# Performance work log

Hardware: AMD Instinct MI355X
Metric: run time of the kernel (lower is better)

## Reference

```python
import jax, jax.numpy as jnp
import numpy as np

H = 512
V = 32000
B = 64
S = 64
T = 64
SOS = 0


def setup_inputs() -> dict:
    key = jax.random.key(0)
    ks = jax.random.split(key, 20)
    s = 1.0 / np.sqrt(H)
    return {
        "encoder_outputs": jax.random.normal(ks[0], (B, S, H), jnp.float32),
        "encoder_hidden": jax.random.normal(ks[1], (1, B, H), jnp.float32),
        "target_tensor": jax.random.randint(ks[2], (B, T), 0, V),
        "emb": jax.random.normal(ks[3], (V, H), jnp.float32) * s,
        "Wa": jax.random.normal(ks[4], (H, H), jnp.float32) * s,
        "ba": jnp.zeros((H,), jnp.float32),
        "Ua": jax.random.normal(ks[5], (H, H), jnp.float32) * s,
        "bu": jnp.zeros((H,), jnp.float32),
        "Va": jax.random.normal(ks[6], (1, H), jnp.float32) * s,
        "bv": jnp.zeros((1,), jnp.float32),
        "W_ih": jax.random.normal(ks[7], (3 * H, 2 * H), jnp.float32) * s,
        "W_hh": jax.random.normal(ks[8], (3 * H, H), jnp.float32) * s,
        "b_ih": jnp.zeros((3 * H,), jnp.float32),
        "b_hh": jnp.zeros((3 * H,), jnp.float32),
        "W_out": jax.random.normal(ks[9], (V, H), jnp.float32) * s,
        "b_out": jnp.zeros((V,), jnp.float32),
    }


def reference(encoder_outputs, encoder_hidden, target_tensor, emb, Wa, ba, Ua, bu,
              Va, bv, W_ih, W_hh, b_ih, b_hh, W_out, b_out):
    # Teacher-forced inputs: SOS then target[:, :-1]
    sos = jnp.full((B, 1), SOS, dtype=target_tensor.dtype)
    inputs = jnp.concatenate([sos, target_tensor[:, :-1]], axis=1)  # [B,T]
    emb_seq = emb[inputs]  # [B,T,H]

    # Precompute Ua(keys): invariant across decode steps
    Uk = jnp.einsum('bsh,kh->bsk', encoder_outputs, Ua) + bu  # [B,S,H]
    h0 = encoder_hidden[0]  # [B,H]

    def step(h, x_t):
        # Bahdanau attention: Va * tanh(Wa q + Ua k)
        q = h @ Wa.T + ba                                   # [B,H]
        scores = jnp.tanh(q[:, None, :] + Uk) @ Va[0] + bv[0]  # [B,S]
        w = jax.nn.softmax(scores, axis=-1)                 # [B,S]
        ctx = jnp.einsum('bs,bsh->bh', w, encoder_outputs)  # [B,H]
        # GRU cell (PyTorch gate layout: r, z, n)
        x = jnp.concatenate([x_t, ctx], axis=-1)            # [B,2H]
        gi = x @ W_ih.T + b_ih
        gh = h @ W_hh.T + b_hh
        ir, iz, inn = jnp.split(gi, 3, axis=-1)
        hr, hz, hn = jnp.split(gh, 3, axis=-1)
        r = jax.nn.sigmoid(ir + hr)
        z = jax.nn.sigmoid(iz + hz)
        n = jnp.tanh(inn + r * hn)
        h_new = (1.0 - z) * n + z * h
        logits = h_new @ W_out.T + b_out                    # [B,V]
        return h_new, (logits, w)

    hT, (logits, attn) = jax.lax.scan(step, h0, jnp.swapaxes(emb_seq, 0, 1))
    log_probs = jax.nn.log_softmax(jnp.swapaxes(logits, 0, 1), axis=-1)  # [B,T,V]
    attentions = jnp.swapaxes(attn, 0, 1)                                # [B,T,S]
    return log_probs, hT[None], attentions
```

## Files before the change

### kernel.cpp

```cpp
#include <hip/hip_runtime.h>
#include <math.h>

#define HH 512
#define VV 32000
#define BB 64
#define SS 64
#define TT 64
#define H3 1536

#define WS_GIEMBBF 0LL
#define WS_UKBF    3145728LL
#define WS_ENCBF   4194304LL
#define WS_EMBBF   5242880LL
#define WS_WCATBF  6291456LL
#define WS_WIHC3   6815744LL
#define WS_WIHE    7208960LL
#define WS_UABF    7602176LL
#define WS_BCAT    7733248LL
#define WS_QGH     7735296LL
#define WS_CTXBF   7866368LL
#define WS_H32     7882752LL
#define WS_HBF     7948288LL
#define WS_HSALL   8388608LL

#define OUT_HT  ((long long)BB*TT*VV)
#define OUT_ATT (OUT_HT + (long long)BB*HH)

typedef __attribute__((ext_vector_type(8))) short bf16x8;
typedef __attribute__((ext_vector_type(4))) float f32x4;

__device__ inline unsigned short f2b(float x) {
  unsigned u = __builtin_bit_cast(unsigned, x);
  unsigned r = (u + 0x7FFF + ((u >> 16) & 1)) >> 16;
  return (unsigned short)r;
}
__device__ inline float bc(unsigned u) { return __builtin_bit_cast(float, u); }
__device__ inline float b2f(unsigned short h) { return bc(((unsigned)h) << 16); }
__device__ inline float frcp(float x) { return __builtin_amdgcn_rcpf(x); }
__device__ inline float tanh_fast(float x) { return 1.f - 2.f * frcp(__expf(2.f * x) + 1.f); }
__device__ inline float sigm(float x) { return frcp(1.f + __expf(-x)); }

#define GLDS(gp, lp) __builtin_amdgcn_global_load_lds( \
    (const __attribute__((address_space(1))) void*)(gp), \
    (__attribute__((address_space(3))) void*)(lp), 16, 0, 0)

__global__ __launch_bounds__(256) void build_wcat_kernel(const float* __restrict__ Wa,
    const float* __restrict__ Whh, const float* __restrict__ ba,
    const float* __restrict__ bhh, unsigned short* __restrict__ wcatbf,
    float* __restrict__ bcat)
{
  long long i = (long long)blockIdx.x * 256 + threadIdx.x;
  int j = (int)(i >> 9), k = (int)(i & 511);
  float v = (j < HH) ? Wa[(long long)j*HH + k] : Whh[(long long)(j - HH)*HH + k];
  wcatbf[i] = f2b(v);
  if (i < 2048) bcat[i] = (i < HH) ? ba[i] : bhh[i - HH];
}

__global__ __launch_bounds__(256) void build_wihc3_kernel(const float* __restrict__ W_ih,
    unsigned short* __restrict__ o)
{
  long long i = (long long)blockIdx.x * 256 + threadIdx.x;
  int rp = (int)(i >> 9), k = (int)(i & 511);
  int j = rp / 3, g = rp - j * 3;
  o[i] = f2b(W_ih[((long long)(g*512 + j))*1024 + 512 + k]);
}

__global__ __launch_bounds__(256) void build_wihe_kernel(const float* __restrict__ W_ih,
    unsigned short* __restrict__ o)
{
  long long i = (long long)blockIdx.x * 256 + threadIdx.x;
  o[i] = f2b(W_ih[(long long)(i >> 9)*1024 + (i & 511)]);
}

__global__ __launch_bounds__(256) void cvt_f2b_kernel(const float* __restrict__ in,
    unsigned short* __restrict__ outp, long long n)
{
  long long i = ((long long)blockIdx.x * 256 + threadIdx.x) * 4;
  if (i >= n) return;
  float4 v = *(const float4*)(in + i);
  ushort4 r = { f2b(v.x), f2b(v.y), f2b(v.z), f2b(v.w) };
  *(ushort4*)(outp + i) = r;
}

__global__ __launch_bounds__(256) void build_embbf_kernel(const float* __restrict__ emb,
    const int* __restrict__ tgt, unsigned short* __restrict__ embbf)
{
  const int m = blockIdx.x, t = m >> 6, b = m & 63;
  const int tk = (t == 0) ? 0 : tgt[b*TT + t - 1];
  const float* src = emb + (long long)tk*HH;
  unsigned short* dst = embbf + (long long)m*HH;
  const int i = threadIdx.x;
  dst[i] = f2b(src[i]);
  dst[i + 256] = f2b(src[i + 256]);
}

__global__ __launch_bounds__(256) void hinit_kernel(const float* __restrict__ eh,
    unsigned short* __restrict__ hbf0, float* __restrict__ h320)
{
  int i = blockIdx.x * 256 + threadIdx.x;
  float v = eh[i];
  hbf0[i] = f2b(v);
  h320[i] = v;
}

template<int OUTBF>
__global__ __launch_bounds__(256) void mfma_nt(const unsigned short* __restrict__ A,
    const unsigned short* __restrict__ Bw, const float* __restrict__ bias,
    void* __restrict__ Cv, long long ldc)
{
  __shared__ unsigned short As[128*32];
  __shared__ unsigned short Bs[128*32];
  const int tid = threadIdx.x;
  const int w = tid >> 6, l = tid & 63;
  const int m0 = blockIdx.y * 128, n0 = blockIdx.x * 128;
  const int wr = w >> 1, wc = w & 1;

  f32x4 acc[4][4];
  #pragma unroll
  for (int i = 0; i < 4; i++)
    #pragma unroll
    for (int j = 0; j < 4; j++) acc[i][j] = (f32x4){0.f, 0.f, 0.f, 0.f};

  const int srow = l >> 2;
  const int scol = (l & 3) * 8;

  for (int k0 = 0; k0 < HH; k0 += 32) {
    __syncthreads();
    #pragma unroll
    for (int q = 0; q < 2; ++q) {
      int r = w*32 + q*16 + srow;
      GLDS(A  + (long long)(m0 + r)*HH + k0 + scol, As + r*32 + scol);
      GLDS(Bw + (long long)(n0 + r)*HH + k0 + scol, Bs + r*32 + scol);
    }
    __syncthreads();

    bf16x8 a[4], b[4];
    #pragma unroll
    for (int mi = 0; mi < 4; mi++)
      a[mi] = *(const bf16x8*)&As[(wr*64 + mi*16 + (l & 15))*32 + (l >> 4)*8];
    #pragma unroll
    for (int ni = 0; ni < 4; ni++)
      b[ni] = *(const bf16x8*)&Bs[(wc*64 + ni*16 + (l & 15))*32 + (l >> 4)*8];
    #pragma unroll
    for (int mi = 0; mi < 4; mi++)
      #pragma unroll
      for (int ni = 0; ni < 4; ni++)
        acc[mi][ni] = __builtin_amdgcn_mfma_f32_16x16x32_bf16(a[mi], b[ni], acc[mi][ni], 0, 0, 0);
  }

  #pragma unroll
  for (int mi = 0; mi < 4; mi++) {
    #pragma unroll
    for (int ni = 0; ni < 4; ni++) {
      int col = n0 + wc*64 + ni*16 + (l & 15);
      float bb = bias[col];
      #pragma unroll
      for (int r2 = 0; r2 < 4; r2++) {
        int row = m0 + wr*64 + mi*16 + (l >> 4)*4 + r2;
        float v = acc[mi][ni][r2] + bb;
        if (OUTBF) ((unsigned short*)Cv)[(long long)row*ldc + col] = f2b(v);
        else       ((float*)Cv)[(long long)row*ldc + col] = v;
      }
    }
  }
}

__global__ __launch_bounds__(256) void qgh_mfma(
    const unsigned short* __restrict__ hbf_r, const unsigned short* __restrict__ wcatbf,
    const float* __restrict__ bcat, float* __restrict__ qgh)
{
  __shared__ unsigned short As[64*32];
  __shared__ unsigned short Bs[128*32];
  const int tid = threadIdx.x;
  const int w = tid >> 6, l = tid & 63;
  const int n0 = blockIdx.x * 128;
  const int wr = w >> 1, wc = w & 1;

  f32x4 acc[2][4];
  #pragma unroll
  for (int i = 0; i < 2; i++)
    #pragma unroll
    for (int j = 0; j < 4; j++) acc[i][j] = (f32x4){0.f, 0.f, 0.f, 0.f};

  const int ar = tid >> 2;
  const int ac8 = (tid & 3) * 8;

  for (int k0 = 0; k0 < HH; k0 += 32) {
    __syncthreads();
    GLDS(hbf_r + (long long)ar*HH + k0 + ac8, As + ar*32 + ac8);
    #pragma unroll
    for (int q = 0; q < 2; ++q) {
      int r = q*64 + ar;
      GLDS(wcatbf + (long long)(n0 + r)*HH + k0 + ac8, Bs + r*32 + ac8);
    }
    __syncthreads();

    bf16x8 a[2], b[4];
    #pragma unroll
    for (int mi = 0; mi < 2; mi++)
      a[mi] = *(const bf16x8*)&As[(wr*32 + mi*16 + (l & 15))*32 + (l >> 4)*8];
    #pragma unroll
    for (int ni = 0; ni < 4; ni++)
      b[ni] = *(const bf16x8*)&Bs[(wc*64 + ni*16 + (l & 15))*32 + (l >> 4)*8];
    #pragma unroll
    for (int mi = 0; mi < 2; mi++)
      #pragma unroll
      for (int ni = 0; ni < 4; ni++)
        acc[mi][ni] = __builtin_amdgcn_mfma_f32_16x16x32_bf16(a[mi], b[ni], acc[mi][ni], 0, 0, 0);
  }

  #pragma unroll
  for (int mi = 0; mi < 2; mi++) {
    #pragma unroll
    for (int ni = 0; ni < 4; ni++) {
      int col = n0 + wc*64 + ni*16 + (l & 15);
      float bb = bcat[col];
      #pragma unroll
      for (int r2 = 0; r2 < 4; r2++) {
        int row = wr*32 + mi*16 + (l >> 4)*4 + r2;
        qgh[(long long)row*2048 + col] = acc[mi][ni][r2] + bb;
      }
    }
  }
}

__global__ __launch_bounds__(512) void attn_kernel(int t,
    const float* __restrict__ qgh, const unsigned short* __restrict__ ukbf,
    const unsigned short* __restrict__ encbf, const float* __restrict__ Va,
    const float* __restrict__ bvp,
    unsigned short* __restrict__ ctxbf, float* __restrict__ attn_out)
{
  const int b = blockIdx.x, tid = threadIdx.x;
  __shared__ float qs2[8][68];
  __shared__ float vsh[8][68];
  __shared__ float sc[SS], sw[SS];

  qs2[tid >> 6][tid & 63] = qgh[(long long)b*2048 + tid];
  vsh[tid >> 6][tid & 63] = Va[tid];
  __syncthreads();

  {
    const int s = tid >> 3, sub = tid & 7;
    const uint4* up = (const uint4*)(ukbf + ((long long)(b*SS + s))*512 + sub*64);
    const float* qp = &qs2[sub][0];
    const float* vp = &vsh[sub][0];
    float p_ = 0.f;
    #pragma unroll
    for (int i = 0; i < 8; ++i) {
      uint4 uv = up[i];
      int e = i*8;
      p_ = fmaf(vp[e+0], tanh_fast(qp[e+0] + bc(uv.x << 16)), p_);
      p_ = fmaf(vp[e+1], tanh_fast(qp[e+1] + bc(uv.x & 0xffff0000u)), p_);
      p_ = fmaf(vp[e+2], tanh_fast(qp[e+2] + bc(uv.y << 16)), p_);
      p_ = fmaf(vp[e+3], tanh_fast(qp[e+3] + bc(uv.y & 0xffff0000u)), p_);
      p_ = fmaf(vp[e+4], tanh_fast(qp[e+4] + bc(uv.z << 16)), p_);
      p_ = fmaf(vp[e+5], tanh_fast(qp[e+5] + bc(uv.z & 0xffff0000u)), p_);
      p_ = fmaf(vp[e+6], tanh_fast(qp[e+6] + bc(uv.w << 16)), p_);
      p_ = fmaf(vp[e+7], tanh_fast(qp[e+7] + bc(uv.w & 0xffff0000u)), p_);
    }
    p_ += __shfl_xor(p_, 1);
    p_ += __shfl_xor(p_, 2);
    p_ += __shfl_xor(p_, 4);
    if (sub == 0) sc[s] = p_ + bvp[0];
  }
  __syncthreads();

  if (tid < 64) {
    float x = sc[tid], mx = x;
    #pragma unroll
    for (int off = 32; off; off >>= 1) mx = fmaxf(mx, __shfl_xor(mx, off));
    float e = __expf(x - mx), sm = e;
    #pragma unroll
    for (int off = 32; off; off >>= 1) sm += __shfl_xor(sm, off);
    float w_ = e * frcp(sm);
    sw[tid] = w_;
    attn_out[((long long)b*TT + t)*SS + tid] = w_;
  }
  __syncthreads();

  {
    float a = 0.f;
    const unsigned short* ep = encbf + (long long)b*SS*512 + tid;
    #pragma unroll 8
    for (int s = 0; s < SS; ++s)
      a = fmaf(sw[s], b2f(ep[s*512]), a);
    ctxbf[b*512 + tid] = f2b(a);
  }
}

__global__ __launch_bounds__(256) void gic_gates_mfma(int t,
    const unsigned short* __restrict__ ctxbf, const unsigned short* __restrict__ wihc3bf,
    const float* __restrict__ qgh, const unsigned short* __restrict__ giembbf,
    const float* __restrict__ h32_r, float* __restrict__ h32_w,
    unsigned short* __restrict__ hbf_w, unsigned short* __restrict__ hsall,
    float* __restrict__ out_ht)
{
  __shared__ unsigned short As[64*32];
  __shared__ unsigned short Bs[96*32];
  __shared__ float gl[64*100];
  const int tid = threadIdx.x;
  const int w = tid >> 6, l = tid & 63;
  const int n0 = blockIdx.x * 96, j0 = blockIdx.x * 32;
  const int wr = w >> 1, wc = w & 1;

  f32x4 acc[2][3];
  #pragma unroll
  for (int i = 0; i < 2; i++)
    #pragma unroll
    for (int j = 0; j < 3; j++) acc[i][j] = (f32x4){0.f, 0.f, 0.f, 0.f};

  const int ar = tid >> 2;
  const int ac8 = (tid & 3) * 8;

  for (int k0 = 0; k0 < HH; k0 += 32) {
    __syncthreads();
    GLDS(ctxbf + (long long)ar*HH + k0 + ac8, As + ar*32 + ac8);
    #pragma unroll
    for (int q = 0; q < 2; ++q) {
      int idx = tid + q*256;
      if (idx < 384) {
        int r = idx >> 2, c8 = (idx & 3) * 8;
        GLDS(wihc3bf + (long long)(n0 + r)*HH + k0 + c8, Bs + r*32 + c8);
      }
    }
    __syncthreads();

    bf16x8 a[2], b[3];
    #pragma unroll
    for (int mi = 0; mi < 2; mi++)
      a[mi] = *(const bf16x8*)&As[(wr*32 + mi*16 + (l & 15))*32 + (l >> 4)*8];
    #pragma unroll
    for (int ni = 0; ni < 3; ni++)
      b[ni] = *(const bf16x8*)&Bs[(wc*48 + ni*16 + (l & 15))*32 + (l >> 4)*8];
    #pragma unroll
    for (int mi = 0; mi < 2; mi++)
      #pragma unroll
      for (int ni = 0; ni < 3; ni++)
        acc[mi][ni] = __builtin_amdgcn_mfma_f32_16x16x32_bf16(a[mi], b[ni], acc[mi][ni], 0, 0, 0);
  }

  #pragma unroll
  for (int mi = 0; mi < 2; mi++)
    #pragma unroll
    for (int ni = 0; ni < 3; ni++) {
      int col = wc*48 + ni*16 + (l & 15);
      #pragma unroll
      for (int r2 = 0; r2 < 4; r2++) {
        int row = wr*32 + mi*16 + (l >> 4)*4 + r2;
        gl[row*100 + col] = acc[mi][ni][r2];
      }
    }
  __syncthreads();

  for (int i = tid; i < 2048; i += 256) {
    const int b = i >> 5, jj = i & 31, j = j0 + jj;
    float gr = gl[b*100 + jj*3 + 0];
    float gz = gl[b*100 + jj*3 + 1];
    float gn = gl[b*100 + jj*3 + 2];
    const float* qg = qgh + (long long)b*2048 + 512;
    float ghr = qg[j], ghz = qg[512 + j], ghn = qg[1024 + j];
    const long long gb = ((long long)t*BB + b)*H3 + j;
    float gir = b2f(giembbf[gb]);
    float giz = b2f(giembbf[gb + 512]);
    float gin = b2f(giembbf[gb + 1024]);
    float r = sigm(gir + gr + ghr);
    float z = sigm(giz + gz + ghz);
    float n = tanh_fast(gin + gn + r * ghn);
    float hold = h32_r[b*512 + j];
    float hn = (1.f - z) * n + z * hold;
    h32_w[b*512 + j] = hn;
    unsigned short hb = f2b(hn);
    hbf_w[b*512 + j] = hb;
    hsall[((long long)b*TT + t)*512 + j] = hb;
    if (t == TT - 1) out_ht[b*512 + j] = hn;
  }
}

__global__ __launch_bounds__(1024) void logsoftmax_kernel(float* __restrict__ lp)
{
  float4* p4 = (float4*)(lp + (long long)blockIdx.x * VV);
  const int tid = threadIdx.x;
  float m = -1e30f, s = 0.f;
  for (int v = tid; v < 8000; v += 1024) {
    float4 x = p4[v];
    float mx = fmaxf(fmaxf(x.x, x.y), fmaxf(x.z, x.w));
    float e = __expf(x.x - mx) + __expf(x.y - mx) + __expf(x.z - mx) + __expf(x.w - mx);
    if (mx > m) { s = s * __expf(m - mx) + e; m = mx; }
    else        { s += e * __expf(mx - m); }
  }
  #pragma unroll
  for (int off = 32; off; off >>= 1) {
    float m2 = __shfl_xor(m, off), s2 = __shfl_xor(s, off);
    float mm = fmaxf(m, m2);
    s = s * __expf(m - mm) + s2 * __expf(m2 - mm);
    m = mm;
  }
  __shared__ float rm[16], rs[16];
  if ((tid & 63) == 0) { rm[tid >> 6] = m; rs[tid >> 6] = s; }
  __syncthreads();
  float M = rm[0], S = rs[0];
  #pragma unroll
  for (int i = 1; i < 16; ++i) {
    float m2 = rm[i], s2 = rs[i];
    float mm = fmaxf(M, m2);
    S = S * __expf(M - mm) + s2 * __expf(m2 - mm);
    M = mm;
  }
  const float L = M + logf(S);
  for (int v = tid; v < 8000; v += 1024) {
    float4 x = p4[v];
    x.x -= L; x.y -= L; x.z -= L; x.w -= L;
    p4[v] = x;
  }
}

extern "C" void kernel_launch(void* const* d_in, const int* in_sizes, int n_in,
                              void* d_out, int out_size, void* d_ws, size_t ws_size,
                              hipStream_t stream)
{
  const float* enc   = (const float*)d_in[0];
  const float* eh    = (const float*)d_in[1];
  const int*   tgt   = (const int*)  d_in[2];
  const float* emb   = (const float*)d_in[3];
  const float* Wa    = (const float*)d_in[4];
  const float* ba    = (const float*)d_in[5];
  const float* Ua    = (const float*)d_in[6];
  const float* bu    = (const float*)d_in[7];
  const float* Va    = (const float*)d_in[8];
  const float* bvp   = (const float*)d_in[9];
  const float* W_ih  = (const float*)d_in[10];
  const float* W_hh  = (const float*)d_in[11];
  const float* b_ih  = (const float*)d_in[12];
  const float* b_hh  = (const float*)d_in[13];
  const float* W_out = (const float*)d_in[14];
  const float* b_out = (const float*)d_in[15];

  float* out = (float*)d_out;
  float* ws  = (float*)d_ws;

  unsigned short* giembbf = (unsigned short*)(ws + WS_GIEMBBF);
  unsigned short* ukbf    = (unsigned short*)(ws + WS_UKBF);
  unsigned short* encbf   = (unsigned short*)(ws + WS_ENCBF);
  unsigned short* embbf   = (unsigned short*)(ws + WS_EMBBF);
  unsigned short* wcatbf  = (unsigned short*)(ws + WS_WCATBF);
  unsigned short* wihc3bf = (unsigned short*)(ws + WS_WIHC3);
  unsigned short* wihebf  = (unsigned short*)(ws + WS_WIHE);
  unsigned short* uabf    = (unsigned short*)(ws + WS_UABF);
  float* bcat = ws + WS_BCAT;
  float* qgh  = ws + WS_QGH;
  unsigned short* ctxbf = (unsigned short*)(ws + WS_CTXBF);
  float* h320 = ws + WS_H32;
  float* h321 = h320 + BB*HH;
  unsigned short* hbf0 = (unsigned short*)(ws + WS_HBF);
  unsigned short* hbf1 = hbf0 + BB*HH;
  unsigned short* hsall = (unsigned short*)(ws + WS_HSALL);
  unsigned short* wbf   = (unsigned short*)ws;

  float* attn_out = out + OUT_ATT;
  float* out_ht   = out + OUT_HT;

  build_wcat_kernel<<<dim3(4096), dim3(256), 0, stream>>>(Wa, W_hh, ba, b_hh, wcatbf, bcat);
  build_wihc3_kernel<<<dim3(3072), dim3(256), 0, stream>>>(W_ih, wihc3bf);
  build_wihe_kernel<<<dim3(3072), dim3(256), 0, stream>>>(W_ih, wihebf);
  cvt_f2b_kernel<<<dim3(256), dim3(256), 0, stream>>>(Ua, uabf, (long long)HH*HH);
  cvt_f2b_kernel<<<dim3(2048), dim3(256), 0, stream>>>(enc, encbf, (long long)BB*SS*HH);
  build_embbf_kernel<<<dim3(4096), dim3(256), 0, stream>>>(emb, tgt, embbf);
  hinit_kernel<<<dim3(128), dim3(256), 0, stream>>>(eh, hbf0, h320);

  mfma_nt<1><<<dim3(4, 32), dim3(256), 0, stream>>>(encbf, uabf, bu, (void*)ukbf, (long long)HH);
  mfma_nt<1><<<dim3(12, 32), dim3(256), 0, stream>>>(embbf, wihebf, b_ih, (void*)giembbf, (long long)H3);

  for (int t = 0; t < TT; ++t) {
    const unsigned short* hr  = (t & 1) ? hbf1 : hbf0;
    const float*          h32r = (t & 1) ? h321 : h320;
    unsigned short*       hw  = (t & 1) ? hbf0 : hbf1;
    float*                h32w = (t & 1) ? h320 : h321;
    qgh_mfma<<<dim3(16), dim3(256), 0, stream>>>(hr, wcatbf, bcat, qgh);
    attn_kernel<<<dim3(64), dim3(512), 0, stream>>>(t, qgh, ukbf, encbf, Va, bvp, ctxbf, attn_out);
    gic_gates_mfma<<<dim3(16), dim3(256), 0, stream>>>(t, ctxbf, wihc3bf, qgh, giembbf,
        h32r, h32w, hw, hsall, out_ht);
  }

  cvt_f2b_kernel<<<dim3(16000), dim3(256), 0, stream>>>(W_out, wbf, (long long)VV*HH);
  mfma_nt<0><<<dim3(250, 32), dim3(256), 0, stream>>>(hsall, wbf, b_out, (void*)out, (long long)VV);
  logsoftmax_kernel<<<dim3(4096), dim3(1024), 0, stream>>>(out);
}
```

Baseline: 2.274 ms.

## Fuse query projection into attention and hidden GEMM into gate kernel

Removes the separate qgh GEMM kernel per decode step. Each attention block now computes its own Wa·h query row with MFMA (re-reading Wa from L2 per batch block). The W_hh·h product moves into the gate kernel using a gate-interleaved bf16 copy of W_hh, so it runs alongside the ctx GEMM. This cuts one launch and a global round trip per step, at the cost of redundant Wa loads across 64 blocks and halved thread count in attention.

New measurement: 2.564 ms. 12.8% more time.

```diff
diff --git a/kernel.cpp b/kernel.cpp
--- a/kernel.cpp
+++ b/kernel.cpp
@@ -16,11 +16,11 @@
 #define WS_WIHC3   6815744LL
 #define WS_WIHE    7208960LL
 #define WS_UABF    7602176LL
-#define WS_BCAT    7733248LL
-#define WS_QGH     7735296LL
-#define WS_CTXBF   7866368LL
-#define WS_H32     7882752LL
-#define WS_HBF     7948288LL
+#define WS_WHH3    7733248LL
+#define WS_BCAT    8126464LL
+#define WS_CTXBF   8128512LL
+#define WS_H32     8144896LL
+#define WS_HBF     8210432LL
 #define WS_HSALL   8388608LL
 
 #define OUT_HT  ((long long)BB*TT*VV)
@@ -56,13 +56,13 @@
   if (i < 2048) bcat[i] = (i < HH) ? ba[i] : bhh[i - HH];
 }
 
-__global__ __launch_bounds__(256) void build_wihc3_kernel(const float* __restrict__ W_ih,
-    unsigned short* __restrict__ o)
+__global__ __launch_bounds__(256) void build_g3_kernel(const float* __restrict__ Wsrc,
+    unsigned short* __restrict__ o, int ld, int ofs)
 {
   long long i = (long long)blockIdx.x * 256 + threadIdx.x;
   int rp = (int)(i >> 9), k = (int)(i & 511);
   int j = rp / 3, g = rp - j * 3;
-  o[i] = f2b(W_ih[((long long)(g*512 + j))*1024 + 512 + k]);
+  o[i] = f2b(Wsrc[((long long)(g*512 + j))*ld + ofs + k]);
 }
 
 __global__ __launch_bounds__(256) void build_wihe_kernel(const float* __restrict__ W_ih,
@@ -165,102 +165,81 @@
   }
 }
 
-__global__ __launch_bounds__(256) void qgh_mfma(
-    const unsigned short* __restrict__ hbf_r, const unsigned short* __restrict__ wcatbf,
-    const float* __restrict__ bcat, float* __restrict__ qgh)
-{
-  __shared__ unsigned short As[64*32];
-  __shared__ unsigned short Bs[128*32];
-  const int tid = threadIdx.x;
-  const int w = tid >> 6, l = tid & 63;
-  const int n0 = blockIdx.x * 128;
-  const int wr = w >> 1, wc = w & 1;
-
-  f32x4 acc[2][4];
-  #pragma unroll
-  for (int i = 0; i < 2; i++)
-    #pragma unroll
-    for (int j = 0; j < 4; j++) acc[i][j] = (f32x4){0.f, 0.f, 0.f, 0.f};
-
-  const int ar = tid >> 2;
-  const int ac8 = (tid & 3) * 8;
-
-  for (int k0 = 0; k0 < HH; k0 += 32) {
-    __syncthreads();
-    GLDS(hbf_r + (long long)ar*HH + k0 + ac8, As + ar*32 + ac8);
-    #pragma unroll
-    for (int q = 0; q < 2; ++q) {
-      int r = q*64 + ar;
-      GLDS(wcatbf + (long long)(n0 + r)*HH + k0 + ac8, Bs + r*32 + ac8);
-    }
-    __syncthreads();
-
-    bf16x8 a[2], b[4];
-    #pragma unroll
-    for (int mi = 0; mi < 2; mi++)
-      a[mi] = *(const bf16x8*)&As[(wr*32 + mi*16 + (l & 15))*32 + (l >> 4)*8];
-    #pragma unroll
-    for (int ni = 0; ni < 4; ni++)
-      b[ni] = *(const bf16x8*)&Bs[(wc*64 + ni*16 + (l & 15))*32 + (l >> 4)*8];
-    #pragma unroll
-    for (int mi = 0; mi < 2; mi++)
-      #pragma unroll
-      for (int ni = 0; ni < 4; ni++)
-        acc[mi][ni] = __builtin_amdgcn_mfma_f32_16x16x32_bf16(a[mi], b[ni], acc[mi][ni], 0, 0, 0);
-  }
-
-  #pragma unroll
-  for (int mi = 0; mi < 2; mi++) {
-    #pragma unroll
-    for (int ni = 0; ni < 4; ni++) {
-      int col = n0 + wc*64 + ni*16 + (l & 15);
-      float bb = bcat[col];
-      #pragma unroll
-      for (int r2 = 0; r2 < 4; r2++) {
-        int row = wr*32 + mi*16 + (l >> 4)*4 + r2;
-        qgh[(long long)row*2048 + col] = acc[mi][ni][r2] + bb;
-      }
-    }
-  }
-}
-
-__global__ __launch_bounds__(512) void attn_kernel(int t,
-    const float* __restrict__ qgh, const unsigned short* __restrict__ ukbf,
+__global__ __launch_bounds__(256) void q_attn_kernel(int t,
+    const unsigned short* __restrict__ hbf_r, const unsigned short* __restrict__ wabf,
+    const float* __restrict__ bcat, const unsigned short* __restrict__ ukbf,
     const unsigned short* __restrict__ encbf, const float* __restrict__ Va,
     const float* __restrict__ bvp,
     unsigned short* __restrict__ ctxbf, float* __restrict__ attn_out)
 {
   const int b = blockIdx.x, tid = threadIdx.x;
+  const int w = tid >> 6, l = tid & 63;
+  __shared__ unsigned short hsh[512];
+  __shared__ unsigned short Ws[512*32];
   __shared__ float qs2[8][68];
   __shared__ float vsh[8][68];
   __shared__ float sc[SS], sw[SS];
 
-  qs2[tid >> 6][tid & 63] = qgh[(long long)b*2048 + tid];
+  ((unsigned*)hsh)[tid] = ((const unsigned*)(hbf_r + (long long)b*512))[tid];
   vsh[tid >> 6][tid & 63] = Va[tid];
+  vsh[(tid + 256) >> 6][tid & 63] = Va[tid + 256];
+  __syncthreads();
+
+  f32x4 acc[8];
+  #pragma unroll
+  for (int i = 0; i < 8; i++) acc[i] = (f32x4){0.f, 0.f, 0.f, 0.f};
+
+  for (int k0 = 0; k0 < HH; k0 += 32) {
+    if (k0) __syncthreads();
+    #pragma unroll
+    for (int q = 0; q < 8; ++q) {
+      int idx = tid + q*256;
+      int r = idx >> 2, c8 = (idx & 3) * 8;
+      GLDS(wabf + (long long)r*HH + k0 + c8, Ws + r*32 + c8);
+    }
+    __syncthreads();
+
+    bf16x8 a = *(const bf16x8*)&hsh[k0 + (l >> 4)*8];
+    #pragma unroll
+    for (int i = 0; i < 8; ++i) {
+      bf16x8 bfr = *(const bf16x8*)&Ws[(w*128 + i*16 + (l & 15))*32 + (l >> 4)*8];
+      acc[i] = __builtin_amdgcn_mfma_f32_16x16x32_bf16(a, bfr, acc[i], 0, 0, 0);
+    }
+  }
+  if (l < 16) {
+    #pragma unroll
+    for (int i = 0; i < 8; ++i) {
+      int col = w*128 + i*16 + l;
+      qs2[col >> 6][col & 63] = acc[i][0] + bcat[col];
+    }
+  }
   __syncthreads();
 
   {
-    const int s = tid >> 3, sub = tid & 7;
-    const uint4* up = (const uint4*)(ukbf + ((long long)(b*SS + s))*512 + sub*64);
-    const float* qp = &qs2[sub][0];
-    const float* vp = &vsh[sub][0];
+    const int s = tid >> 2, sub = tid & 3;
     float p_ = 0.f;
     #pragma unroll
-    for (int i = 0; i < 8; ++i) {
-      uint4 uv = up[i];
-      int e = i*8;
-      p_ = fmaf(vp[e+0], tanh_fast(qp[e+0] + bc(uv.x << 16)), p_);
-      p_ = fmaf(vp[e+1], tanh_fast(qp[e+1] + bc(uv.x & 0xffff0000u)), p_);
-      p_ = fmaf(vp[e+2], tanh_fast(qp[e+2] + bc(uv.y << 16)), p_);
-      p_ = fmaf(vp[e+3], tanh_fast(qp[e+3] + bc(uv.y & 0xffff0000u)), p_);
-      p_ = fmaf(vp[e+4], tanh_fast(qp[e+4] + bc(uv.z << 16)), p_);
-      p_ = fmaf(vp[e+5], tanh_fast(qp[e+5] + bc(uv.z & 0xffff0000u)), p_);
-      p_ = fmaf(vp[e+6], tanh_fast(qp[e+6] + bc(uv.w << 16)), p_);
-      p_ = fmaf(vp[e+7], tanh_fast(qp[e+7] + bc(uv.w & 0xffff0000u)), p_);
+    for (int half = 0; half < 2; ++half) {
+      const int row = sub*2 + half;
+      const uint4* up = (const uint4*)(ukbf + ((long long)(b*SS + s))*512 + row*64);
+      const float* qp = &qs2[row][0];
+      const float* vp = &vsh[row][0];
+      #pragma unroll
+      for (int i = 0; i < 8; ++i) {
+        uint4 uv = up[i];
+        int e = i*8;
+        p_ = fmaf(vp[e+0], tanh_fast(qp[e+0] + bc(uv.x << 16)), p_);
+        p_ = fmaf(vp[e+1], tanh_fast(qp[e+1] + bc(uv.x & 0xffff0000u)), p_);
+        p_ = fmaf(vp[e+2], tanh_fast(qp[e+2] + bc(uv.y << 16)), p_);
+        p_ = fmaf(vp[e+3], tanh_fast(qp[e+3] + bc(uv.y & 0xffff0000u)), p_);
+        p_ = fmaf(vp[e+4], tanh_fast(qp[e+4] + bc(uv.z << 16)), p_);
+        p_ = fmaf(vp[e+5], tanh_fast(qp[e+5] + bc(uv.z & 0xffff0000u)), p_);
+        p_ = fmaf(vp[e+6], tanh_fast(qp[e+6] + bc(uv.w << 16)), p_);
+        p_ = fmaf(vp[e+7], tanh_fast(qp[e+7] + bc(uv.w & 0xffff0000u)), p_);
+      }
     }
     p_ += __shfl_xor(p_, 1);
     p_ += __shfl_xor(p_, 2);
-    p_ += __shfl_xor(p_, 4);
     if (sub == 0) sc[s] = p_ + bvp[0];
   }
   __syncthreads();
@@ -279,64 +258,86 @@
   __syncthreads();
 
   {
-    float a = 0.f;
-    const unsigned short* ep = encbf + (long long)b*SS*512 + tid;
+    float a0 = 0.f, a1 = 0.f;
+    const unsigned short* ep = encbf + (long long)b*SS*512;
     #pragma unroll 8
-    for (int s = 0; s < SS; ++s)
-      a = fmaf(sw[s], b2f(ep[s*512]), a);
-    ctxbf[b*512 + tid] = f2b(a);
-  }
-}
-
-__global__ __launch_bounds__(256) void gic_gates_mfma(int t,
-    const unsigned short* __restrict__ ctxbf, const unsigned short* __restrict__ wihc3bf,
-    const float* __restrict__ qgh, const unsigned short* __restrict__ giembbf,
+    for (int s = 0; s < SS; ++s) {
+      float w_ = sw[s];
+      a0 = fmaf(w_, b2f(ep[s*512 + tid]), a0);
+      a1 = fmaf(w_, b2f(ep[s*512 + tid + 256]), a1);
+    }
+    ctxbf[b*512 + tid]       = f2b(a0);
+    ctxbf[b*512 + tid + 256] = f2b(a1);
+  }
+}
+
+__global__ __launch_bounds__(256) void ghgic_gates_mfma(int t,
+    const unsigned short* __restrict__ hbf_r, const unsigned short* __restrict__ ctxbf,
+    const unsigned short* __restrict__ wihc3bf, const unsigned short* __restrict__ whh3bf,
+    const float* __restrict__ bcat, const unsigned short* __restrict__ giembbf,
     const float* __restrict__ h32_r, float* __restrict__ h32_w,
     unsigned short* __restrict__ hbf_w, unsigned short* __restrict__ hsall,
     float* __restrict__ out_ht)
 {
   __shared__ unsigned short As[64*32];
+  __shared__ unsigned short Hs[64*32];
   __shared__ unsigned short Bs[96*32];
+  __shared__ unsigned short Cs[96*32];
   __shared__ float gl[64*100];
+  __shared__ float hl[64*100];
   const int tid = threadIdx.x;
   const int w = tid >> 6, l = tid & 63;
   const int n0 = blockIdx.x * 96, j0 = blockIdx.x * 32;
   const int wr = w >> 1, wc = w & 1;
 
-  f32x4 acc[2][3];
+  f32x4 accg[2][3], acch[2][3];
   #pragma unroll
   for (int i = 0; i < 2; i++)
     #pragma unroll
-    for (int j = 0; j < 3; j++) acc[i][j] = (f32x4){0.f, 0.f, 0.f, 0.f};
-
-  const int ar = tid >> 2;
-  const int ac8 = (tid & 3) * 8;
+    for (int j = 0; j < 3; j++) {
+      accg[i][j] = (f32x4){0.f, 0.f, 0.f, 0.f};
+      acch[i][j] = (f32x4){0.f, 0.f, 0.f, 0.f};
+    }
 
   for (int k0 = 0; k0 < HH; k0 += 32) {
     __syncthreads();
-    GLDS(ctxbf + (long long)ar*HH + k0 + ac8, As + ar*32 + ac8);
-    #pragma unroll
-    for (int q = 0; q < 2; ++q) {
+    #pragma unroll
+    for (int q = 0; q < 5; ++q) {
       int idx = tid + q*256;
-      if (idx < 384) {
+      if (idx < 256) {
         int r = idx >> 2, c8 = (idx & 3) * 8;
+        GLDS(ctxbf + (long long)r*HH + k0 + c8, As + r*32 + c8);
+      } else if (idx < 512) {
+        int i2 = idx - 256, r = i2 >> 2, c8 = (i2 & 3) * 8;
+        GLDS(hbf_r + (long long)r*HH + k0 + c8, Hs + r*32 + c8);
+      } else if (idx < 896) {
+        int i2 = idx - 512, r = i2 >> 2, c8 = (i2 & 3) * 8;
         GLDS(wihc3bf + (long long)(n0 + r)*HH + k0 + c8, Bs + r*32 + c8);
+      } else {
+        int i2 = idx - 896, r = i2 >> 2, c8 = (i2 & 3) * 8;
+        GLDS(whh3bf + (long long)(n0 + r)*HH + k0 + c8, Cs + r*32 + c8);
       }
     }
     __syncthreads();
 
-    bf16x8 a[2], b[3];
-    #pragma unroll
-    for (int mi = 0; mi < 2; mi++)
-      a[mi] = *(const bf16x8*)&As[(wr*32 + mi*16 + (l & 15))*32 + (l >> 4)*8];
-    #pragma unroll
-    for (int ni = 0; ni < 3; ni++)
-      b[ni] = *(const bf16x8*)&Bs[(wc*48 + ni*16 + (l & 15))*32 + (l >> 4)*8];
+    bf16x8 ag[2], ah[2], bg[3], bh[3];
+    #pragma unroll
+    for (int mi = 0; mi < 2; mi++) {
+      ag[mi] = *(const bf16x8*)&As[(wr*32 + mi*16 + (l & 15))*32 + (l >> 4)*8];
+      ah[mi] = *(const bf16x8*)&Hs[(wr*32 + mi*16 + (l & 15))*32 + (l >> 4)*8];
+    }
+    #pragma unroll
+    for (int ni = 0; ni < 3; ni++) {
+      bg[ni] = *(const bf16x8*)&Bs[(wc*48 + ni*16 + (l & 15))*32 + (l >> 4)*8];
+      bh[ni] = *(const bf16x8*)&Cs[(wc*48 + ni*16 + (l & 15))*32 + (l >> 4)*8];
+    }
     #pragma unroll
     for (int mi = 0; mi < 2; mi++)
       #pragma unroll
-      for (int ni = 0; ni < 3; ni++)
-        acc[mi][ni] = __builtin_amdgcn_mfma_f32_16x16x32_bf16(a[mi], b[ni], acc[mi][ni], 0, 0, 0);
+      for (int ni = 0; ni < 3; ni++) {
+        accg[mi][ni] = __builtin_amdgcn_mfma_f32_16x16x32_bf16(ag[mi], bg[ni], accg[mi][ni], 0, 0, 0);
+        acch[mi][ni] = __builtin_amdgcn_mfma_f32_16x16x32_bf16(ah[mi], bh[ni], acch[mi][ni], 0, 0, 0);
+      }
   }
 
   #pragma unroll
@@ -347,25 +348,27 @@
       #pragma unroll
       for (int r2 = 0; r2 < 4; r2++) {
         int row = wr*32 + mi*16 + (l >> 4)*4 + r2;
-        gl[row*100 + col] = acc[mi][ni][r2];
+        gl[row*100 + col] = accg[mi][ni][r2];
+        hl[row*100 + col] = acch[mi][ni][r2];
       }
     }
   __syncthreads();
 
   for (int i = tid; i < 2048; i += 256) {
     const int b = i >> 5, jj = i & 31, j = j0 + jj;
-    float gr = gl[b*100 + jj*3 + 0];
-    float gz = gl[b*100 + jj*3 + 1];
-    float gn = gl[b*100 + jj*3 + 2];
-    const float* qg = qgh + (long long)b*2048 + 512;
-    float ghr = qg[j], ghz = qg[512 + j], ghn = qg[1024 + j];
+    float gcr = gl[b*100 + jj*3 + 0];
+    float gcz = gl[b*100 + jj*3 + 1];
+    float gcn = gl[b*100 + jj*3 + 2];
+    float ghr = hl[b*100 + jj*3 + 0] + bcat[512 + j];
+    float ghz = hl[b*100 + jj*3 + 1] + bcat[1024 + j];
+    float ghn = hl[b*100 + jj*3 + 2] + bcat[1536 + j];
     const long long gb = ((long long)t*BB + b)*H3 + j;
     float gir = b2f(giembbf[gb]);
     float giz = b2f(giembbf[gb + 512]);
     float gin = b2f(giembbf[gb + 1024]);
-    float r = sigm(gir + gr + ghr);
-    float z = sigm(giz + gz + ghz);
-    float n = tanh_fast(gin + gn + r * ghn);
+    float r = sigm(gir + gcr + ghr);
+    float z = sigm(giz + gcz + ghz);
+    float n = tanh_fast(gin + gcn + r * ghn);
     float hold = h32_r[b*512 + j];
     float hn = (1.f - z) * n + z * hold;
     h32_w[b*512 + j] = hn;
@@ -446,8 +449,8 @@
   unsigned short* wihc3bf = (unsigned short*)(ws + WS_WIHC3);
   unsigned short* wihebf  = (unsigned short*)(ws + WS_WIHE);
   unsigned short* uabf    = (unsigned short*)(ws + WS_UABF);
+  unsigned short* whh3bf  = (unsigned short*)(ws + WS_WHH3);
   float* bcat = ws + WS_BCAT;
-  float* qgh  = ws + WS_QGH;
   unsigned short* ctxbf = (unsigned short*)(ws + WS_CTXBF);
   float* h320 = ws + WS_H32;
   float* h321 = h320 + BB*HH;
@@ -460,7 +463,8 @@
   float* out_ht   = out + OUT_HT;
 
   build_wcat_kernel<<<dim3(4096), dim3(256), 0, stream>>>(Wa, W_hh, ba, b_hh, wcatbf, bcat);
-  build_wihc3_kernel<<<dim3(3072), dim3(256), 0, stream>>>(W_ih, wihc3bf);
+  build_g3_kernel<<<dim3(3072), dim3(256), 0, stream>>>(W_ih, wihc3bf, 1024, 512);
+  build_g3_kernel<<<dim3(3072), dim3(256), 0, stream>>>(W_hh, whh3bf, 512, 0);
   build_wihe_kernel<<<dim3(3072), dim3(256), 0, stream>>>(W_ih, wihebf);
   cvt_f2b_kernel<<<dim3(256), dim3(256), 0, stream>>>(Ua, uabf, (long long)HH*HH);
   cvt_f2b_kernel<<<dim3(2048), dim3(256), 0, stream>>>(enc, encbf, (long long)BB*SS*HH);
@@ -475,10 +479,10 @@
     const float*          h32r = (t & 1) ? h321 : h320;
     unsigned short*       hw  = (t & 1) ? hbf0 : hbf1;
     float*                h32w = (t & 1) ? h320 : h321;
-    qgh_mfma<<<dim3(16), dim3(256), 0, stream>>>(hr, wcatbf, bcat, qgh);
-    attn_kernel<<<dim3(64), dim3(512), 0, stream>>>(t, qgh, ukbf, encbf, Va, bvp, ctxbf, attn_out);
-    gic_gates_mfma<<<dim3(16), dim3(256), 0, stream>>>(t, ctxbf, wihc3bf, qgh, giembbf,
-        h32r, h32w, hw, hsall, out_ht);
+    q_attn_kernel<<<dim3(64), dim3(256), 0, stream>>>(t, hr, wcatbf, bcat,
+        ukbf, encbf, Va, bvp, ctxbf, attn_out);
+    ghgic_gates_mfma<<<dim3(16), dim3(256), 0, stream>>>(t, hr, ctxbf, wihc3bf, whh3bf,
+        bcat, giembbf, h32r, h32w, hw, hsall, out_ht);
   }
 
   cvt_f2b_kernel<<<dim3(16000), dim3(256), 0, stream>>>(W_out, wbf, (long long)VV*HH);
```
